# Kernel tuning notes

Hardware: AMD Instinct MI355X
Metric: run time of the kernel (lower is better)

## Reference

```python
import jax, jax.numpy as jnp
import numpy as np

THETA = 10000.0

def _rope(x, theta):
    # x: [B, H, S, dh]; interleaved-pair rotary embedding with positions 0..S-1
    B, H, S, dh = x.shape
    inv_freq = theta ** (-jnp.arange(0, dh, 2, dtype=x.dtype) / dh)  # [dh/2]
    ang = jnp.arange(S, dtype=x.dtype)[:, None] * inv_freq[None, :]  # [S, dh/2]
    cos, sin = jnp.cos(ang), jnp.sin(ang)
    x1, x2 = x[..., 0::2], x[..., 1::2]                              # [B,H,S,dh/2]
    r1 = x1 * cos - x2 * sin
    r2 = x1 * sin + x2 * cos
    return jnp.stack([r1, r2], axis=-1).reshape(x.shape)


def setup_inputs() -> dict:
    key = jax.random.key(0)
    ks = jax.random.split(key, 5)
    B, S, D = 4, 2048, 1024
    scale = 1.0 / np.sqrt(D)
    return {
        "x": jax.random.normal(ks[0], (B, S, D), dtype=jnp.float32),
        "Wq": jax.random.normal(ks[1], (D, D), dtype=jnp.float32) * scale,
        "Wk": jax.random.normal(ks[2], (D, D), dtype=jnp.float32) * scale,
        "Wv": jax.random.normal(ks[3], (D, D), dtype=jnp.float32) * scale,
        "Wo": jax.random.normal(ks[4], (D, D), dtype=jnp.float32) * scale,
        "num_heads": 16,
    }


def reference(x, Wq, Wk, Wv, Wo, num_heads):
    B, S, D = x.shape
    H = num_heads
    dh = D // H
    # projections: LinearWeights does x @ W.T
    def split_heads(t):
        return t.reshape(B, S, H, dh).transpose(0, 2, 1, 3)  # [B,H,S,dh]
    q = split_heads(x @ Wq.T)
    k = split_heads(x @ Wk.T)
    v = split_heads(x @ Wv.T)
    q = _rope(q, THETA)
    k = _rope(k, THETA)
    scores = jnp.einsum("bhqd,bhkd->bhqk", q, k) / jnp.sqrt(jnp.asarray(dh, x.dtype))
    causal = jnp.tril(jnp.ones((S, S), dtype=bool))
    scores = jnp.where(causal, scores, jnp.asarray(-1e9, x.dtype))
    attn = jax.nn.softmax(scores, axis=-1)
    out = jnp.einsum("bhqk,bhkd->bhqd", attn, v)      # [B,H,S,dh]
    out = out.transpose(0, 2, 1, 3).reshape(B, S, D)  # merge heads
    return out @ Wo.T
```

## Files before the change

### kernel.cpp

```cpp
#include <hip/hip_runtime.h>
#include <cstddef>
#include <cstdint>

#define S_LEN  2048
#define DMODEL 1024
#define NHEAD  16
#define DHEAD  64

typedef __attribute__((ext_vector_type(8))) short bf16x8;
typedef __attribute__((ext_vector_type(4))) float f32x4;

__device__ __forceinline__ short f2bf(float f) {
  unsigned u = __float_as_uint(f);
  u += 0x7fffu + ((u >> 16) & 1u);
  return (short)(u >> 16);
}

#define SW(row, byteInRow) ((((row) << 7) + (byteInRow)) ^ (((row) & 7) << 4))

__global__ void rope_table_kernel(float* __restrict__ cosT, float* __restrict__ sinT) {
  const int idx = blockIdx.x * blockDim.x + threadIdx.x;
  if (idx >= S_LEN * 32) return;
  const int s = idx >> 5;
  const int i = idx & 31;
  const float inv = powf(10000.0f, -(float)(2 * i) / (float)DHEAD);
  const float a = (float)s * inv;
  cosT[idx] = cosf(a);
  sinT[idx] = sinf(a);
}

__global__ __launch_bounds__(256) void convert_kernel(
    const float* __restrict__ x,  const float* __restrict__ wq,
    const float* __restrict__ wk, const float* __restrict__ wv,
    const float* __restrict__ wo,
    unsigned short* __restrict__ xb,  unsigned short* __restrict__ wqb,
    unsigned short* __restrict__ wkb, unsigned short* __restrict__ wvb,
    unsigned short* __restrict__ wob) {
  const int blk = blockIdx.x;
  const float* src;
  unsigned short* dst;
  size_t base;
  if (blk < 4096)      { src = x;  dst = xb;  base = (size_t)blk * 2048; }
  else if (blk < 4608) { src = wq; dst = wqb; base = (size_t)(blk - 4096) * 2048; }
  else if (blk < 5120) { src = wk; dst = wkb; base = (size_t)(blk - 4608) * 2048; }
  else if (blk < 5632) { src = wv; dst = wvb; base = (size_t)(blk - 5120) * 2048; }
  else                 { src = wo; dst = wob; base = (size_t)(blk - 5632) * 2048; }
  const size_t o = base + (size_t)threadIdx.x * 8;
  const float4 v0 = *(const float4*)(src + o);
  const float4 v1 = *(const float4*)(src + o + 4);
  bf16x8 p;
  p[0] = f2bf(v0.x); p[1] = f2bf(v0.y); p[2] = f2bf(v0.z); p[3] = f2bf(v0.w);
  p[4] = f2bf(v1.x); p[5] = f2bf(v1.y); p[6] = f2bf(v1.z); p[7] = f2bf(v1.w);
  *(bf16x8*)(dst + o) = p;
}

#define GEMM_CORE(A_, W_, mBase_, nBase_)                                          \
  f32x4 acc[4][4] = {};                                                            \
  for (int kb = 0; kb < DMODEL; kb += 64) {                                        \
    bf16x8 ar[4], br[4];                                                           \
    _Pragma("unroll")                                                              \
    for (int i = 0; i < 4; ++i) {                                                  \
      const int qd  = t + (i << 8);                                                \
      const int row = qd >> 3;                                                     \
      const int sl  = qd & 7;                                                      \
      ar[i] = *(const bf16x8*)(A_ + (size_t)(mBase_ + row) * DMODEL + kb + (sl << 3)); \
      br[i] = *(const bf16x8*)(W_ + (size_t)(nBase_ + row) * DMODEL + kb + (sl << 3)); \
    }                                                                              \
    __syncthreads();                                                               \
    _Pragma("unroll")                                                              \
    for (int i = 0; i < 4; ++i) {                                                  \
      const int qd  = t + (i << 8);                                                \
      const int row = qd >> 3;                                                     \
      const int sl  = qd & 7;                                                      \
      const int off = ((row << 7) + (sl << 4)) ^ ((row & 7) << 4);                 \
      *(bf16x8*)((char*)As + off) = ar[i];                                         \
      *(bf16x8*)((char*)Bs + off) = br[i];                                         \
    }                                                                              \
    __syncthreads();                                                               \
    _Pragma("unroll")                                                              \
    for (int ks = 0; ks < 2; ++ks) {                                               \
      const int kof = (ks << 6) + (rg << 4);                                       \
      bf16x8 af[4], bfr[4];                                                        \
      _Pragma("unroll")                                                            \
      for (int mf = 0; mf < 4; ++mf) {                                             \
        const int r = (wm << 6) + (mf << 4) + cl;                                  \
        af[mf] = *(const bf16x8*)((const char*)As + (((r << 7) + kof) ^ ((r & 7) << 4))); \
      }                                                                            \
      _Pragma("unroll")                                                            \
      for (int nf = 0; nf < 4; ++nf) {                                             \
        const int r = (wn << 6) + (nf << 4) + cl;                                  \
        bfr[nf] = *(const bf16x8*)((const char*)Bs + (((r << 7) + kof) ^ ((r & 7) << 4))); \
      }                                                                            \
      _Pragma("unroll")                                                            \
      for (int mf = 0; mf < 4; ++mf)                                               \
        _Pragma("unroll")                                                          \
        for (int nf = 0; nf < 4; ++nf)                                             \
          acc[mf][nf] = __builtin_amdgcn_mfma_f32_16x16x32_bf16(af[mf], bfr[nf], acc[mf][nf], 0, 0, 0); \
    }                                                                              \
  }

__global__ __launch_bounds__(256) void gemm_qkv(
    const unsigned short* __restrict__ A,
    const unsigned short* __restrict__ Wqb, const unsigned short* __restrict__ Wkb,
    const unsigned short* __restrict__ Wvb,
    unsigned short* __restrict__ Qo, unsigned short* __restrict__ Ko,
    unsigned short* __restrict__ Vo,
    const float* __restrict__ cosT, const float* __restrict__ sinT) {
  __shared__ short As[128 * 64];
  __shared__ short Bs[128 * 64];
  const int t    = threadIdx.x;
  const int lane = t & 63;
  const int w    = t >> 6;
  const int wm   = w >> 1, wn = w & 1;
  const int cl   = lane & 15;
  const int rg   = lane >> 4;
  const int mBase = blockIdx.x << 7;
  const int nSel  = blockIdx.y >> 3;
  const int nBase = (blockIdx.y & 7) << 7;
  const unsigned short* W = (nSel == 0) ? Wqb : (nSel == 1) ? Wkb : Wvb;

  GEMM_CORE(A, W, mBase, nBase)

  if (nSel < 2) {
    unsigned short* out = (nSel == 0) ? Qo : Ko;
    const int h = (nBase >> 6) + wn;
#pragma unroll
    for (int nf = 0; nf < 4; ++nf) {
      const int d    = (nf << 4) + cl;
      const int pi   = d >> 1;
      const bool odd = d & 1;
#pragma unroll
      for (int mf = 0; mf < 4; ++mf) {
#pragma unroll
        for (int r = 0; r < 4; ++r) {
          const int m = mBase + (wm << 6) + (mf << 4) + (rg << 2) + r;
          const int s = m & (S_LEN - 1);
          const int b = m >> 11;
          float v = acc[mf][nf][r];
          const float other = __shfl_xor(v, 1);
          const float c  = cosT[(s << 5) + pi];
          const float sn = sinT[(s << 5) + pi];
          v = v * c + (odd ? other * sn : -other * sn);
          out[((size_t)(b * NHEAD + h) * S_LEN + s) * DHEAD + d] = (unsigned short)f2bf(v);
        }
      }
    }
  } else {
    typedef __attribute__((ext_vector_type(4))) short bf16x4;
    const int h = (nBase >> 6) + wn;
#pragma unroll
    for (int mf = 0; mf < 4; ++mf) {
      const int m0 = mBase + (wm << 6) + (mf << 4) + (rg << 2);
      const int s0 = m0 & (S_LEN - 1);
      const int b  = m0 >> 11;
#pragma unroll
      for (int nf = 0; nf < 4; ++nf) {
        const int d = (nf << 4) + cl;
        bf16x4 pk;
        pk[0] = f2bf(acc[mf][nf][0]); pk[1] = f2bf(acc[mf][nf][1]);
        pk[2] = f2bf(acc[mf][nf][2]); pk[3] = f2bf(acc[mf][nf][3]);
        *(bf16x4*)(Vo + ((size_t)(b * NHEAD + h) * DHEAD + d) * S_LEN + s0) = pk;
      }
    }
  }
}

__global__ __launch_bounds__(256) void gemm_plain(
    const unsigned short* __restrict__ A, const unsigned short* __restrict__ W,
    float* __restrict__ out) {
  __shared__ short As[128 * 64];
  __shared__ short Bs[128 * 64];
  const int t    = threadIdx.x;
  const int lane = t & 63;
  const int w    = t >> 6;
  const int wm   = w >> 1, wn = w & 1;
  const int cl   = lane & 15;
  const int rg   = lane >> 4;
  const int mBase = blockIdx.x << 7;
  const int nBase = blockIdx.y << 7;

  GEMM_CORE(A, W, mBase, nBase)

#pragma unroll
  for (int mf = 0; mf < 4; ++mf) {
    const int rowb = mBase + (wm << 6) + (mf << 4) + (rg << 2);
#pragma unroll
    for (int nf = 0; nf < 4; ++nf) {
      const int col = nBase + (wn << 6) + (nf << 4) + cl;
#pragma unroll
      for (int r = 0; r < 4; ++r)
        out[(size_t)(rowb + r) * DMODEL + col] = acc[mf][nf][r];
    }
  }
}

__global__ __launch_bounds__(256) void attn_mfma(const unsigned short* __restrict__ Qbf,
                                                 const unsigned short* __restrict__ Kbf,
                                                 const unsigned short* __restrict__ VTbf,
                                                 unsigned short* __restrict__ O) {
  __shared__ short Qs[64 * 64];
  __shared__ short Ks[64 * 64];
  __shared__ short Vs[64 * 64];
  __shared__ short Ps[64 * 64];
  const int t    = threadIdx.x;
  const int lane = t & 63;
  const int w    = t >> 6;
  const int cl   = lane & 15;
  const int rg   = lane >> 4;
  const int qw   = w << 4;
  const int bh   = blockIdx.y;
  const int p    = blockIdx.x;
  const int b    = bh >> 4, h = bh & 15;

  const unsigned short* kbase = Kbf + (size_t)bh * S_LEN * DHEAD;
  const unsigned short* vbase = VTbf + (size_t)bh * DHEAD * S_LEN;

  const int srow  = t >> 2;
  const int sslot = t & 3;

  for (int pass = 0; pass < 2; ++pass) {
    const int qt = pass ? (31 - p) : p;
    const int q0 = qt << 6;

    {
      const int qrow = qw + (lane >> 2);
      const int qsl  = lane & 3;
      const unsigned short* qp =
          Qbf + ((size_t)bh * S_LEN + q0 + qrow) * DHEAD + (qsl << 4);
      const bf16x8 qa = *(const bf16x8*)qp;
      const bf16x8 qb = *(const bf16x8*)(qp + 8);
      asm volatile("s_waitcnt lgkmcnt(0)" ::: "memory");
      *(bf16x8*)((char*)Qs + SW(qrow, (qsl << 5)))      = qa;
      *(bf16x8*)((char*)Qs + SW(qrow, (qsl << 5) + 16)) = qb;
    }

    f32x4 oacc[4];
#pragma unroll
    for (int nf = 0; nf < 4; ++nf) oacc[nf] = (f32x4){0.f, 0.f, 0.f, 0.f};
    float m_run[4], l_run[4];
#pragma unroll
    for (int r = 0; r < 4; ++r) { m_run[r] = -3.0e38f; l_run[r] = 0.0f; }

    for (int tk = 0; tk <= qt; ++tk) {
      const int kv0 = tk << 6;
      const unsigned short* kp = kbase + (size_t)(kv0 + srow) * DHEAD + (sslot << 4);
      const unsigned short* vp = vbase + (size_t)srow * S_LEN + kv0 + (sslot << 4);
      const bf16x8 k0 = *(const bf16x8*)kp;
      const bf16x8 k1 = *(const bf16x8*)(kp + 8);
      const bf16x8 v0 = *(const bf16x8*)vp;
      const bf16x8 v1 = *(const bf16x8*)(vp + 8);
      __syncthreads();
      *(bf16x8*)((char*)Ks + SW(srow, (sslot << 5)))      = k0;
      *(bf16x8*)((char*)Ks + SW(srow, (sslot << 5) + 16)) = k1;
      *(bf16x8*)((char*)Vs + SW(srow, (sslot << 5)))      = v0;
      *(bf16x8*)((char*)Vs + SW(srow, (sslot << 5) + 16)) = v1;
      __syncthreads();

      f32x4 sfrag[4];
#pragma unroll
      for (int nf = 0; nf < 4; ++nf) sfrag[nf] = (f32x4){0.f, 0.f, 0.f, 0.f};
#pragma unroll
      for (int ks = 0; ks < 2; ++ks) {
        const bf16x8 aq = *(const bf16x8*)((const char*)Qs + SW(qw + cl, (ks << 6) + (rg << 4)));
#pragma unroll
        for (int nf = 0; nf < 4; ++nf) {
          const bf16x8 bk = *(const bf16x8*)((const char*)Ks + SW((nf << 4) + cl, (ks << 6) + (rg << 4)));
          sfrag[nf] = __builtin_amdgcn_mfma_f32_16x16x32_bf16(aq, bk, sfrag[nf], 0, 0, 0);
        }
      }

      const bool diag = (tk == qt);
      float esc4[4];
#pragma unroll
      for (int r = 0; r < 4; ++r) {
        const int qg = q0 + qw + (rg << 2) + r;
        float sv[4];
#pragma unroll
        for (int nf = 0; nf < 4; ++nf) {
          float x = sfrag[nf][r] * 0.125f;
          if (diag && (kv0 + (nf << 4) + cl > qg)) x = -1.0e9f;
          sv[nf] = x;
        }
        float tm = fmaxf(fmaxf(sv[0], sv[1]), fmaxf(sv[2], sv[3]));
        tm = fmaxf(tm, __shfl_xor(tm, 1));
        tm = fmaxf(tm, __shfl_xor(tm, 2));
        tm = fmaxf(tm, __shfl_xor(tm, 4));
        tm = fmaxf(tm, __shfl_xor(tm, 8));
        const float mn  = fmaxf(m_run[r], tm);
        const float esc = __expf(m_run[r] - mn);
        m_run[r] = mn;
        float rs = 0.0f;
        unsigned short pb[4];
#pragma unroll
        for (int nf = 0; nf < 4; ++nf) {
          const float pv = __expf(sv[nf] - mn);
          rs += pv;
          pb[nf] = (unsigned short)f2bf(pv);
        }
        rs += __shfl_xor(rs, 1);
        rs += __shfl_xor(rs, 2);
        rs += __shfl_xor(rs, 4);
        rs += __shfl_xor(rs, 8);
        l_run[r] = l_run[r] * esc + rs;
        esc4[r] = esc;
        const int prow = qw + (rg << 2) + r;
#pragma unroll
        for (int nf = 0; nf < 4; ++nf)
          *(unsigned short*)((char*)Ps + SW(prow, (nf << 5) + (cl << 1))) = pb[nf];
      }

#pragma unroll
      for (int nf = 0; nf < 4; ++nf)
#pragma unroll
        for (int r = 0; r < 4; ++r) oacc[nf][r] *= esc4[r];

      asm volatile("s_waitcnt lgkmcnt(0)" ::: "memory");

#pragma unroll
      for (int ks = 0; ks < 2; ++ks) {
        const bf16x8 ap = *(const bf16x8*)((const char*)Ps + SW(qw + cl, (ks << 6) + (rg << 4)));
#pragma unroll
        for (int nf = 0; nf < 4; ++nf) {
          const bf16x8 bv = *(const bf16x8*)((const char*)Vs + SW((nf << 4) + cl, (ks << 6) + (rg << 4)));
          oacc[nf] = __builtin_amdgcn_mfma_f32_16x16x32_bf16(ap, bv, oacc[nf], 0, 0, 0);
        }
      }
    }

#pragma unroll
    for (int r = 0; r < 4; ++r) {
      const float inv = 1.0f / l_run[r];
      const int sg = q0 + qw + (rg << 2) + r;
      unsigned short* orow = O + ((size_t)b * S_LEN + sg) * DMODEL + h * DHEAD;
#pragma unroll
      for (int nf = 0; nf < 4; ++nf)
        orow[(nf << 4) + cl] = (unsigned short)f2bf(oacc[nf][r] * inv);
    }
  }
}

extern "C" void kernel_launch(void* const* d_in, const int* in_sizes, int n_in,
                              void* d_out, int out_size, void* d_ws, size_t ws_size,
                              hipStream_t stream) {
  const float* x  = (const float*)d_in[0];
  const float* Wq = (const float*)d_in[1];
  const float* Wk = (const float*)d_in[2];
  const float* Wv = (const float*)d_in[3];
  const float* Wo = (const float*)d_in[4];

  unsigned short* xbf  = (unsigned short*)d_ws;
  unsigned short* Wqb  = xbf + (size_t)8388608;
  unsigned short* Wkb  = Wqb + (size_t)1048576;
  unsigned short* Wvb  = Wkb + (size_t)1048576;
  unsigned short* Wob  = Wvb + (size_t)1048576;
  unsigned short* Qbf  = Wob + (size_t)1048576;
  unsigned short* Kbf  = Qbf + (size_t)8388608;
  unsigned short* VTbf = Kbf + (size_t)8388608;
  unsigned short* Awbf = VTbf + (size_t)8388608;
  float* cosT = (float*)(Awbf + (size_t)8388608);
  float* sinT = cosT + 65536;

  rope_table_kernel<<<256, 256, 0, stream>>>(cosT, sinT);
  convert_kernel<<<6144, 256, 0, stream>>>(x, Wq, Wk, Wv, Wo, xbf, Wqb, Wkb, Wvb, Wob);

  gemm_qkv<<<dim3(64, 24), 256, 0, stream>>>(xbf, Wqb, Wkb, Wvb, Qbf, Kbf, VTbf, cosT, sinT);

  attn_mfma<<<dim3(16, 64), 256, 0, stream>>>(Qbf, Kbf, VTbf, Awbf);

  gemm_plain<<<dim3(64, 8), 256, 0, stream>>>(Awbf, Wob, (float*)d_out);
}
```

Baseline: 314.2 us.

## Use direct global-to-LDS loads in GEMMs and double-buffer K/V in attention

```diff
diff --git a/kernel.cpp b/kernel.cpp
--- a/kernel.cpp
+++ b/kernel.cpp
@@ -18,15 +18,10 @@
 
 #define SW(row, byteInRow) ((((row) << 7) + (byteInRow)) ^ (((row) & 7) << 4))
 
-__global__ void rope_table_kernel(float* __restrict__ cosT, float* __restrict__ sinT) {
-  const int idx = blockIdx.x * blockDim.x + threadIdx.x;
-  if (idx >= S_LEN * 32) return;
-  const int s = idx >> 5;
-  const int i = idx & 31;
-  const float inv = powf(10000.0f, -(float)(2 * i) / (float)DHEAD);
-  const float a = (float)s * inv;
-  cosT[idx] = cosf(a);
-  sinT[idx] = sinf(a);
+__device__ __forceinline__ void gload_lds16(const void* g, void* l) {
+  __builtin_amdgcn_global_load_lds(
+      (const __attribute__((address_space(1))) void*)g,
+      (__attribute__((address_space(3))) void*)l, 16, 0, 0);
 }
 
 __global__ __launch_bounds__(256) void convert_kernel(
@@ -35,8 +30,19 @@
     const float* __restrict__ wo,
     unsigned short* __restrict__ xb,  unsigned short* __restrict__ wqb,
     unsigned short* __restrict__ wkb, unsigned short* __restrict__ wvb,
-    unsigned short* __restrict__ wob) {
+    unsigned short* __restrict__ wob,
+    float* __restrict__ cosT, float* __restrict__ sinT) {
   const int blk = blockIdx.x;
+  if (blk >= 6144) {
+    const int idx = ((blk - 6144) << 8) + threadIdx.x;
+    const int s = idx >> 5;
+    const int i = idx & 31;
+    const float inv = powf(10000.0f, -(float)(2 * i) / (float)DHEAD);
+    const float a = (float)s * inv;
+    cosT[idx] = cosf(a);
+    sinT[idx] = sinf(a);
+    return;
+  }
   const float* src;
   unsigned short* dst;
   size_t base;
@@ -54,49 +60,41 @@
   *(bf16x8*)(dst + o) = p;
 }
 
-#define GEMM_CORE(A_, W_, mBase_, nBase_)                                          \
-  f32x4 acc[4][4] = {};                                                            \
-  for (int kb = 0; kb < DMODEL; kb += 64) {                                        \
-    bf16x8 ar[4], br[4];                                                           \
-    _Pragma("unroll")                                                              \
-    for (int i = 0; i < 4; ++i) {                                                  \
-      const int qd  = t + (i << 8);                                                \
-      const int row = qd >> 3;                                                     \
-      const int sl  = qd & 7;                                                      \
-      ar[i] = *(const bf16x8*)(A_ + (size_t)(mBase_ + row) * DMODEL + kb + (sl << 3)); \
-      br[i] = *(const bf16x8*)(W_ + (size_t)(nBase_ + row) * DMODEL + kb + (sl << 3)); \
-    }                                                                              \
-    __syncthreads();                                                               \
-    _Pragma("unroll")                                                              \
-    for (int i = 0; i < 4; ++i) {                                                  \
-      const int qd  = t + (i << 8);                                                \
-      const int row = qd >> 3;                                                     \
-      const int sl  = qd & 7;                                                      \
-      const int off = ((row << 7) + (sl << 4)) ^ ((row & 7) << 4);                 \
-      *(bf16x8*)((char*)As + off) = ar[i];                                         \
-      *(bf16x8*)((char*)Bs + off) = br[i];                                         \
-    }                                                                              \
-    __syncthreads();                                                               \
-    _Pragma("unroll")                                                              \
-    for (int ks = 0; ks < 2; ++ks) {                                               \
-      const int kof = (ks << 6) + (rg << 4);                                       \
-      bf16x8 af[4], bfr[4];                                                        \
-      _Pragma("unroll")                                                            \
-      for (int mf = 0; mf < 4; ++mf) {                                             \
-        const int r = (wm << 6) + (mf << 4) + cl;                                  \
+#define GEMM_CORE_DMA(A_, W_, mBase_, nBase_)                                   \
+  f32x4 acc[4][4] = {};                                                         \
+  for (int kb = 0; kb < DMODEL; kb += 64) {                                     \
+    __syncthreads();          \
+    _Pragma("unroll")                                                           \
+    for (int c = 0; c < 4; ++c) {                                               \
+      const int g   = (w << 2) + c;                                             \
+      const int row = (g << 3) + (lane >> 3);                                   \
+      const int ss  = (lane & 7) ^ (row & 7);                                   \
+      gload_lds16(A_ + (size_t)(mBase_ + row) * DMODEL + kb + (ss << 3),        \
+                  (char*)As + (g << 10));                                       \
+      gload_lds16(W_ + (size_t)(nBase_ + row) * DMODEL + kb + (ss << 3),        \
+                  (char*)Bs + (g << 10));                                       \
+    }                                                                           \
+    __syncthreads();          \
+    _Pragma("unroll")                                                           \
+    for (int ks = 0; ks < 2; ++ks) {                                            \
+      const int kof = (ks << 6) + (rg << 4);                                    \
+      bf16x8 af[4], bfr[4];                                                     \
+      _Pragma("unroll")                                                         \
+      for (int mf = 0; mf < 4; ++mf) {                                          \
+        const int r = (wm << 6) + (mf << 4) + cl;                               \
         af[mf] = *(const bf16x8*)((const char*)As + (((r << 7) + kof) ^ ((r & 7) << 4))); \
-      }                                                                            \
-      _Pragma("unroll")                                                            \
-      for (int nf = 0; nf < 4; ++nf) {                                             \
-        const int r = (wn << 6) + (nf << 4) + cl;                                  \
+      }                                                                         \
+      _Pragma("unroll")                                                         \
+      for (int nf = 0; nf < 4; ++nf) {                                          \
+        const int r = (wn << 6) + (nf << 4) + cl;                               \
         bfr[nf] = *(const bf16x8*)((const char*)Bs + (((r << 7) + kof) ^ ((r & 7) << 4))); \
-      }                                                                            \
-      _Pragma("unroll")                                                            \
-      for (int mf = 0; mf < 4; ++mf)                                               \
-        _Pragma("unroll")                                                          \
-        for (int nf = 0; nf < 4; ++nf)                                             \
+      }                                                                         \
+      _Pragma("unroll")                                                         \
+      for (int mf = 0; mf < 4; ++mf)                                            \
+        _Pragma("unroll")                                                       \
+        for (int nf = 0; nf < 4; ++nf)                                          \
           acc[mf][nf] = __builtin_amdgcn_mfma_f32_16x16x32_bf16(af[mf], bfr[nf], acc[mf][nf], 0, 0, 0); \
-    }                                                                              \
+    }                                                                           \
   }
 
 __global__ __launch_bounds__(256) void gemm_qkv(
@@ -119,7 +117,7 @@
   const int nBase = (blockIdx.y & 7) << 7;
   const unsigned short* W = (nSel == 0) ? Wqb : (nSel == 1) ? Wkb : Wvb;
 
-  GEMM_CORE(A, W, mBase, nBase)
+  GEMM_CORE_DMA(A, W, mBase, nBase)
 
   if (nSel < 2) {
     unsigned short* out = (nSel == 0) ? Qo : Ko;
@@ -179,7 +177,7 @@
   const int mBase = blockIdx.x << 7;
   const int nBase = blockIdx.y << 7;
 
-  GEMM_CORE(A, W, mBase, nBase)
+  GEMM_CORE_DMA(A, W, mBase, nBase)
 
 #pragma unroll
   for (int mf = 0; mf < 4; ++mf) {
@@ -198,9 +196,7 @@
                                                  const unsigned short* __restrict__ Kbf,
                                                  const unsigned short* __restrict__ VTbf,
                                                  unsigned short* __restrict__ O) {
-  __shared__ short Qs[64 * 64];
-  __shared__ short Ks[64 * 64];
-  __shared__ short Vs[64 * 64];
+  __shared__ short KVs[2][2][64 * 64];
   __shared__ short Ps[64 * 64];
   const int t    = threadIdx.x;
   const int lane = t & 63;
@@ -215,24 +211,31 @@
   const unsigned short* kbase = Kbf + (size_t)bh * S_LEN * DHEAD;
   const unsigned short* vbase = VTbf + (size_t)bh * DHEAD * S_LEN;
 
-  const int srow  = t >> 2;
-  const int sslot = t & 3;
+#define STAGE_KV(bb, kv0_)                                                     \
+  {                                                                            \
+    _Pragma("unroll")                                                          \
+    for (int c = 0; c < 2; ++c) {                                              \
+      const int g   = (w << 1) + c;                                            \
+      const int row = (g << 3) + (lane >> 3);                                  \
+      const int ss  = (lane & 7) ^ (row & 7);                                  \
+      gload_lds16(kbase + (size_t)((kv0_) + row) * DHEAD + (ss << 3),          \
+                  (char*)(KVs[bb][0]) + (g << 10));                            \
+      gload_lds16(vbase + (size_t)row * S_LEN + (kv0_) + (ss << 3),            \
+                  (char*)(KVs[bb][1]) + (g << 10));                            \
+    }                                                                          \
+  }
+
+  int cur = 0;
 
   for (int pass = 0; pass < 2; ++pass) {
     const int qt = pass ? (31 - p) : p;
     const int q0 = qt << 6;
 
-    {
-      const int qrow = qw + (lane >> 2);
-      const int qsl  = lane & 3;
-      const unsigned short* qp =
-          Qbf + ((size_t)bh * S_LEN + q0 + qrow) * DHEAD + (qsl << 4);
-      const bf16x8 qa = *(const bf16x8*)qp;
-      const bf16x8 qb = *(const bf16x8*)(qp + 8);
-      asm volatile("s_waitcnt lgkmcnt(0)" ::: "memory");
-      *(bf16x8*)((char*)Qs + SW(qrow, (qsl << 5)))      = qa;
-      *(bf16x8*)((char*)Qs + SW(qrow, (qsl << 5) + 16)) = qb;
-    }
+    const unsigned short* qrow = Qbf + ((size_t)bh * S_LEN + q0 + qw + cl) * DHEAD + (rg << 3);
+    const bf16x8 aq0 = *(const bf16x8*)qrow;
+    const bf16x8 aq1 = *(const bf16x8*)(qrow + 32);
+
+    STAGE_KV(cur, 0)
 
     f32x4 oacc[4];
 #pragma unroll
@@ -243,28 +246,25 @@
 
     for (int tk = 0; tk <= qt; ++tk) {
       const int kv0 = tk << 6;
-      const unsigned short* kp = kbase + (size_t)(kv0 + srow) * DHEAD + (sslot << 4);
-      const unsigned short* vp = vbase + (size_t)srow * S_LEN + kv0 + (sslot << 4);
-      const bf16x8 k0 = *(const bf16x8*)kp;
-      const bf16x8 k1 = *(const bf16x8*)(kp + 8);
-      const bf16x8 v0 = *(const bf16x8*)vp;
-      const bf16x8 v1 = *(const bf16x8*)(vp + 8);
-      __syncthreads();
-      *(bf16x8*)((char*)Ks + SW(srow, (sslot << 5)))      = k0;
-      *(bf16x8*)((char*)Ks + SW(srow, (sslot << 5) + 16)) = k1;
-      *(bf16x8*)((char*)Vs + SW(srow, (sslot << 5)))      = v0;
-      *(bf16x8*)((char*)Vs + SW(srow, (sslot << 5) + 16)) = v1;
-      __syncthreads();
+      if (tk < qt) {
+        STAGE_KV(cur ^ 1, kv0 + 64)
+        asm volatile("s_waitcnt vmcnt(4)" ::: "memory");
+      } else {
+        asm volatile("s_waitcnt vmcnt(0)" ::: "memory");
+      }
+      __builtin_amdgcn_s_barrier();
+      const short* Kb = KVs[cur][0];
+      const short* Vb = KVs[cur][1];
 
       f32x4 sfrag[4];
 #pragma unroll
       for (int nf = 0; nf < 4; ++nf) sfrag[nf] = (f32x4){0.f, 0.f, 0.f, 0.f};
 #pragma unroll
       for (int ks = 0; ks < 2; ++ks) {
-        const bf16x8 aq = *(const bf16x8*)((const char*)Qs + SW(qw + cl, (ks << 6) + (rg << 4)));
+        const bf16x8 aq = ks ? aq1 : aq0;
 #pragma unroll
         for (int nf = 0; nf < 4; ++nf) {
-          const bf16x8 bk = *(const bf16x8*)((const char*)Ks + SW((nf << 4) + cl, (ks << 6) + (rg << 4)));
+          const bf16x8 bk = *(const bf16x8*)((const char*)Kb + SW((nf << 4) + cl, (ks << 6) + (rg << 4)));
           sfrag[nf] = __builtin_amdgcn_mfma_f32_16x16x32_bf16(aq, bk, sfrag[nf], 0, 0, 0);
         }
       }
@@ -273,13 +273,14 @@
       float esc4[4];
 #pragma unroll
       for (int r = 0; r < 4; ++r) {
-        const int qg = q0 + qw + (rg << 2) + r;
         float sv[4];
 #pragma unroll
-        for (int nf = 0; nf < 4; ++nf) {
-          float x = sfrag[nf][r] * 0.125f;
-          if (diag && (kv0 + (nf << 4) + cl > qg)) x = -1.0e9f;
-          sv[nf] = x;
+        for (int nf = 0; nf < 4; ++nf) sv[nf] = sfrag[nf][r] * 0.125f;
+        if (diag) {
+          const int qg = q0 + qw + (rg << 2) + r;
+#pragma unroll
+          for (int nf = 0; nf < 4; ++nf)
+            if (kv0 + (nf << 4) + cl > qg) sv[nf] = -1.0e9f;
         }
         float tm = fmaxf(fmaxf(sv[0], sv[1]), fmaxf(sv[2], sv[3]));
         tm = fmaxf(tm, __shfl_xor(tm, 1));
@@ -321,10 +322,13 @@
         const bf16x8 ap = *(const bf16x8*)((const char*)Ps + SW(qw + cl, (ks << 6) + (rg << 4)));
 #pragma unroll
         for (int nf = 0; nf < 4; ++nf) {
-          const bf16x8 bv = *(const bf16x8*)((const char*)Vs + SW((nf << 4) + cl, (ks << 6) + (rg << 4)));
+          const bf16x8 bv = *(const bf16x8*)((const char*)Vb + SW((nf << 4) + cl, (ks << 6) + (rg << 4)));
           oacc[nf] = __builtin_amdgcn_mfma_f32_16x16x32_bf16(ap, bv, oacc[nf], 0, 0, 0);
         }
       }
+
+      __builtin_amdgcn_s_barrier();
+      cur ^= 1;
     }
 
 #pragma unroll
@@ -337,6 +341,7 @@
         orow[(nf << 4) + cl] = (unsigned short)f2bf(oacc[nf][r] * inv);
     }
   }
+#undef STAGE_KV
 }
 
 extern "C" void kernel_launch(void* const* d_in, const int* in_sizes, int n_in,
@@ -360,8 +365,8 @@
   float* cosT = (float*)(Awbf + (size_t)8388608);
   float* sinT = cosT + 65536;
 
-  rope_table_kernel<<<256, 256, 0, stream>>>(cosT, sinT);
-  convert_kernel<<<6144, 256, 0, stream>>>(x, Wq, Wk, Wv, Wo, xbf, Wqb, Wkb, Wvb, Wob);
+  convert_kernel<<<6400, 256, 0, stream>>>(x, Wq, Wk, Wv, Wo,
+                                           xbf, Wqb, Wkb, Wvb, Wob, cosT, sinT);
 
   gemm_qkv<<<dim3(64, 24), 256, 0, stream>>>(xbf, Wqb, Wkb, Wvb, Qbf, Kbf, VTbf, cosT, sinT);
 
```

Measured after the change: 334.9 us. 6.6% more time.
